# Optimization experiments

Measured on AMD Instinct MI355X. Metric: run time of the kernel, lower is better.

The kernel has to match this reference:

```python
import jax, jax.numpy as jnp
import numpy as np

NUM_QUBITS = 4
NUM_LAYERS = 3


def _ry(state, theta, wire):
    # state: (N,2,2,2,2) real amplitudes; RY(theta) on `wire` (angle scalar or (N,))
    st = jnp.moveaxis(state, wire + 1, -1)
    c = jnp.cos(theta * 0.5)
    s = jnp.sin(theta * 0.5)
    if jnp.ndim(c) == 1:  # per-sample angle -> broadcast over remaining qubit axes
        shape = (c.shape[0],) + (1,) * (st.ndim - 2)
        c = c.reshape(shape)
        s = s.reshape(shape)
    s0, s1 = st[..., 0], st[..., 1]
    new = jnp.stack([c * s0 - s * s1, s * s0 + c * s1], axis=-1)
    return jnp.moveaxis(new, -1, wire + 1)


def _cnot(state, control, target):
    st = jnp.moveaxis(state, (control + 1, target + 1), (-2, -1))
    new = jnp.stack([st[..., 0, :], st[..., 1, ::-1]], axis=-2)
    return jnp.moveaxis(new, (-2, -1), (control + 1, target + 1))


def _circuit(angles, params):
    # angles: (N,4) input rotations; params: (L,4,1) shared variational angles
    N = angles.shape[0]
    state = jnp.zeros((N, 2, 2, 2, 2), angles.dtype).at[:, 0, 0, 0, 0].set(1.0)
    for q in range(NUM_QUBITS):
        state = _ry(state, angles[:, q], q)
    for l in range(NUM_LAYERS):
        for q in range(NUM_QUBITS):
            state = _ry(state, params[l, q, 0], q)
        for q in range(NUM_QUBITS - 1):
            state = _cnot(state, q, q + 1)
    probs = state * state  # amplitudes are real (only RY/CNOT)
    meas = []
    for w in range(NUM_QUBITS):
        axes = tuple(a for a in range(1, NUM_QUBITS + 1) if a != w + 1)
        p = probs.sum(axes)  # (N,2)
        meas.append(p[:, 0] - p[:, 1])  # <Z_w>
    return jnp.stack(meas, axis=-1)  # (N,4)


def setup_inputs() -> dict:
    key = jax.random.key(0)
    k1, k2, k3, k4, k5 = jax.random.split(key, 5)
    B = 8192
    return {
        "x": jax.random.uniform(k1, (B, 1, 28, 28), dtype=jnp.float32),
        "params": jax.random.normal(k2, (NUM_LAYERS, NUM_QUBITS, 1), dtype=jnp.float32),
        "res_w": jax.random.normal(k3, (4, 1, 1, 1), dtype=jnp.float32),
        "cls_w": jax.random.normal(k4, (10, 784), dtype=jnp.float32) * 0.03,
        "cls_b": jax.random.normal(k5, (10,), dtype=jnp.float32) * 0.03,
    }


def reference(x, params, res_w, cls_w, cls_b):
    B = x.shape[0]
    img = x.reshape(B, 28, 28)
    # extract 2x2 patches, element order (r,c),(r,c+1),(r+1,c),(r+1,c+1)
    patches = img.reshape(B, 14, 2, 14, 2).transpose(0, 1, 3, 2, 4).reshape(B, 196, 4)
    # per-patch-index min/max over batch and the 4 elements (matches patch.min()/max())
    mn = patches.min(axis=(0, 2), keepdims=True)
    mx = patches.max(axis=(0, 2), keepdims=True)
    ang = (patches - mn) / (mx - mn + 1e-8) * jnp.pi
    meas = _circuit(ang.reshape(B * 196, 4), params)  # (B*196, 4)
    out = meas.reshape(B, 196 * 4).reshape(B, 4, 14, 14)  # matches torch.cat(...).view
    # res_conv: 1x1 conv, stride 2, no bias -> strided pixel scaled per out-channel
    res = img[:, ::2, ::2][:, None, :, :] * res_w.reshape(1, 4, 1, 1)
    out = out + res
    logits = out.reshape(B, -1) @ cls_w.T + cls_b
    return jax.nn.log_softmax(logits, axis=-1)
```

## Files before the change

### kernel.cpp

```cpp
#include <hip/hip_runtime.h>
#include <math.h>

#define NP 196
#define PI_F 3.14159265358979323846f

__device__ __forceinline__ unsigned fkey(float f) {
  unsigned u = __float_as_uint(f);
  return u ^ ((unsigned)((int)u >> 31) | 0x80000000u);
}
__device__ __forceinline__ float funkey(unsigned k) {
  unsigned u = (k & 0x80000000u) ? (k ^ 0x80000000u) : ~k;
  return __uint_as_float(u);
}

__global__ void __launch_bounds__(256) precompute_kernel(
    const float* __restrict__ params, const float* __restrict__ res_w,
    const float* __restrict__ cls_w, float* __restrict__ U,
    float* __restrict__ W2, unsigned* __restrict__ mn,
    unsigned* __restrict__ mx) {
  const int tid = threadIdx.x;
  if (tid < NP) {
    mn[tid] = 0xFFFFFFFFu;
    mx[tid] = 0u;
  }
  if (tid < 16) {
    float cp[12], sp[12];
#pragma unroll
    for (int l = 0; l < 12; ++l) __sincosf(0.5f * params[l], &sp[l], &cp[l]);
    float st[16];
#pragma unroll
    for (int i = 0; i < 16; ++i) st[i] = 0.f;
    st[tid] = 1.f;
#pragma unroll
    for (int l = 0; l < 3; ++l) {
#pragma unroll
      for (int q = 0; q < 4; ++q) {
        const float cq = cp[l * 4 + q], sq = sp[l * 4 + q];
        const int m = 8 >> q;
#pragma unroll
        for (int idx = 0; idx < 16; ++idx) {
          if (idx & m) continue;
          float v0 = st[idx], v1 = st[idx | m];
          st[idx] = cq * v0 - sq * v1;
          st[idx | m] = sq * v0 + cq * v1;
        }
      }
#pragma unroll
      for (int q = 0; q < 3; ++q) {
        const int mc = 8 >> q, mt = 4 >> q;
#pragma unroll
        for (int idx = 0; idx < 16; ++idx) {
          if ((idx & mc) && !(idx & mt)) {
            float t0 = st[idx];
            st[idx] = st[idx | mt];
            st[idx | mt] = t0;
          }
        }
      }
    }
#pragma unroll
    for (int i = 0; i < 16; ++i) U[i * 16 + tid] = st[i];
  }
  for (int t = tid; t < 10 * NP; t += 256) {
    int k = t / NP, p = t - k * NP;
    float s = 0.f;
#pragma unroll
    for (int c = 0; c < 4; ++c) s += res_w[c] * cls_w[k * 784 + c * NP + p];
    W2[t] = s;
  }
}

__global__ void __launch_bounds__(512) minmax_kernel(
    const float* __restrict__ x, unsigned* __restrict__ mn,
    unsigned* __restrict__ mx, int imgs, int B) {
  __shared__ unsigned skmin[392], skmax[392];
  const int t = threadIdx.x;
  const int img0 = blockIdx.x * imgs;
  if (t < 392) {
    const int r = t / 14, j = t - r * 14;
    const float* base = x + (size_t)img0 * 784 + r * 28 + 2 * j;
    const int nimg = (img0 + imgs <= B) ? imgs : (B - img0);
    float lmn0 = 3.4e38f, lmn1 = 3.4e38f;
    float lmx0 = -3.4e38f, lmx1 = -3.4e38f;
    int m = 0;
#pragma unroll 4
    for (; m + 1 < nimg; m += 2) {
      float2 v0 = *(const float2*)(base + (size_t)m * 784);
      float2 v1 = *(const float2*)(base + (size_t)(m + 1) * 784);
      lmn0 = fminf(lmn0, fminf(v0.x, v0.y));
      lmx0 = fmaxf(lmx0, fmaxf(v0.x, v0.y));
      lmn1 = fminf(lmn1, fminf(v1.x, v1.y));
      lmx1 = fmaxf(lmx1, fmaxf(v1.x, v1.y));
    }
    if (m < nimg) {
      float2 v0 = *(const float2*)(base + (size_t)m * 784);
      lmn0 = fminf(lmn0, fminf(v0.x, v0.y));
      lmx0 = fmaxf(lmx0, fmaxf(v0.x, v0.y));
    }
    skmin[t] = fkey(fminf(lmn0, lmn1));
    skmax[t] = fkey(fmaxf(lmx0, lmx1));
  }
  __syncthreads();
  if (t < NP) {
    const int i = t / 14, j = t - i * 14;
    const int f0 = (2 * i) * 14 + j, f1 = f0 + 14;
    unsigned kmn = skmin[f0] < skmin[f1] ? skmin[f0] : skmin[f1];
    unsigned kmx = skmax[f0] > skmax[f1] ? skmax[f0] : skmax[f1];
    atomicMin(&mn[t], kmn);
    atomicMax(&mx[t], kmx);
  }
}

__global__ void __launch_bounds__(256) fused_kernel(
    const float* __restrict__ x, const unsigned* __restrict__ mnk,
    const unsigned* __restrict__ mxk, const float* __restrict__ U,
    const float* __restrict__ W2, const float* __restrict__ cls_w,
    const float* __restrict__ cls_b, float* __restrict__ out) {
  __shared__ float partial[4][10];

  const int t = threadIdx.x;
  const int b = blockIdx.x;

  float acc[10];
#pragma unroll
  for (int k = 0; k < 10; ++k) acc[k] = 0.f;

  if (t < NP) {
    const int p = t;
    const int i = p / 14, j = p - i * 14;
    const float* px = x + (size_t)b * 784 + (2 * i) * 28 + 2 * j;
    const float2 r0 = *(const float2*)px;
    const float2 r1 = *(const float2*)(px + 28);

    const float mnv = funkey(mnk[p]);
    const float mxv = funkey(mxk[p]);
    const float sc = (0.5f * PI_F) / (mxv - mnv + 1e-8f);

    float cc[4], ss[4];
    __sincosf((r0.x - mnv) * sc, &ss[0], &cc[0]);
    __sincosf((r0.y - mnv) * sc, &ss[1], &cc[1]);
    __sincosf((r1.x - mnv) * sc, &ss[2], &cc[2]);
    __sincosf((r1.y - mnv) * sc, &ss[3], &cc[3]);

    float st0[16];
    {
      const float A[4] = {cc[0] * cc[1], cc[0] * ss[1], ss[0] * cc[1], ss[0] * ss[1]};
      const float Bq[4] = {cc[2] * cc[3], cc[2] * ss[3], ss[2] * cc[3], ss[2] * ss[3]};
#pragma unroll
      for (int idx = 0; idx < 16; ++idx) st0[idx] = A[idx >> 2] * Bq[idx & 3];
    }

    float a8[8], z3 = 0.f;
#pragma unroll
    for (int k = 0; k < 8; ++k) {
      float f0 = 0.f, f1 = 0.f;
#pragma unroll
      for (int jx = 0; jx < 16; ++jx) {
        f0 = fmaf(U[(2 * k) * 16 + jx], st0[jx], f0);
        f1 = fmaf(U[(2 * k + 1) * 16 + jx], st0[jx], f1);
      }
      const float s0 = f0 * f0, s1 = f1 * f1;
      a8[k] = s0 + s1;
      z3 += s0 - s1;
    }
    float bb[4], z2 = 0.f;
#pragma unroll
    for (int k = 0; k < 4; ++k) {
      bb[k] = a8[2 * k] + a8[2 * k + 1];
      z2 += a8[2 * k] - a8[2 * k + 1];
    }
    const float e0 = bb[0] + bb[1], e1 = bb[2] + bb[3];
    const float z1 = (bb[0] - bb[1]) + (bb[2] - bb[3]);
    const float z0 = e0 - e1;
    const float v = r0.x;

#pragma unroll
    for (int k = 0; k < 10; ++k) {
      const float4 w4 = *(const float4*)(cls_w + k * 784 + 4 * p);
      float a = z0 * w4.x;
      a = fmaf(z1, w4.y, a);
      a = fmaf(z2, w4.z, a);
      a = fmaf(z3, w4.w, a);
      acc[k] = fmaf(v, W2[k * NP + p], a);
    }
  }

  const int lane = t & 63, wv = t >> 6;
#pragma unroll
  for (int k = 0; k < 10; ++k) {
    float a = acc[k];
#pragma unroll
    for (int off = 32; off > 0; off >>= 1) a += __shfl_down(a, off, 64);
    if (lane == 0) partial[wv][k] = a;
  }
  __syncthreads();

  if (t == 0) {
    float lg[10];
#pragma unroll
    for (int k = 0; k < 10; ++k)
      lg[k] = partial[0][k] + partial[1][k] + partial[2][k] + partial[3][k] + cls_b[k];
    float m = lg[0];
#pragma unroll
    for (int k = 1; k < 10; ++k) m = fmaxf(m, lg[k]);
    float s = 0.f;
#pragma unroll
    for (int k = 0; k < 10; ++k) s += __expf(lg[k] - m);
    const float lse = m + __logf(s);
#pragma unroll
    for (int k = 0; k < 10; ++k) out[(size_t)b * 10 + k] = lg[k] - lse;
  }
}

extern "C" void kernel_launch(void* const* d_in, const int* in_sizes, int n_in,
                              void* d_out, int out_size, void* d_ws, size_t ws_size,
                              hipStream_t stream) {
  const float* x      = (const float*)d_in[0];
  const float* params = (const float*)d_in[1];
  const float* res_w  = (const float*)d_in[2];
  const float* cls_w  = (const float*)d_in[3];
  const float* cls_b  = (const float*)d_in[4];
  float* out = (float*)d_out;
  const int B = in_sizes[0] / 784;

  unsigned* mn = (unsigned*)d_ws;
  unsigned* mx = mn + NP;
  float* U  = (float*)(mx + NP);
  float* W2 = U + 256;

  precompute_kernel<<<1, 256, 0, stream>>>(params, res_w, cls_w, U, W2, mn, mx);

  const int imgs = 16;
  const int nblk1 = (B + imgs - 1) / imgs;
  minmax_kernel<<<nblk1, 512, 0, stream>>>(x, mn, mx, imgs, B);

  fused_kernel<<<B, 256, 0, stream>>>(x, mn, mx, U, W2, cls_w, cls_b, out);
}
```

Before: 127.1 us.

## Map one image per wavefront in fused kernel, dropping block barrier

The fused kernel now gives each 64-lane wavefront one image and loops over the 196 patches in four strided passes, instead of one 256-thread block per image with 60 idle threads. The cross-wave shared-memory reduction and __syncthreads are removed, since the wave-level shuffle reduction alone yields the logits. The grid shrinks by 4x. This raises lane utilisation and removes the barrier, at the cost of a serial loop per wave (the last pass is mostly idle) and fewer independent blocks.

```diff
diff --git a/kernel.cpp b/kernel.cpp
--- a/kernel.cpp
+++ b/kernel.cpp
@@ -115,91 +115,93 @@
     const float* __restrict__ x, const unsigned* __restrict__ mnk,
     const unsigned* __restrict__ mxk, const float* __restrict__ U,
     const float* __restrict__ W2, const float* __restrict__ cls_w,
-    const float* __restrict__ cls_b, float* __restrict__ out) {
-  __shared__ float partial[4][10];
-
-  const int t = threadIdx.x;
-  const int b = blockIdx.x;
+    const float* __restrict__ cls_b, float* __restrict__ out, int B) {
+  const int lane = threadIdx.x & 63;
+  const int wv = threadIdx.x >> 6;
+  const int b = blockIdx.x * 4 + wv;
+  if (b >= B) return;
+
+  const float* ximg = x + (size_t)b * 784;
 
   float acc[10];
 #pragma unroll
   for (int k = 0; k < 10; ++k) acc[k] = 0.f;
 
-  if (t < NP) {
-    const int p = t;
-    const int i = p / 14, j = p - i * 14;
-    const float* px = x + (size_t)b * 784 + (2 * i) * 28 + 2 * j;
-    const float2 r0 = *(const float2*)px;
-    const float2 r1 = *(const float2*)(px + 28);
-
-    const float mnv = funkey(mnk[p]);
-    const float mxv = funkey(mxk[p]);
-    const float sc = (0.5f * PI_F) / (mxv - mnv + 1e-8f);
-
-    float cc[4], ss[4];
-    __sincosf((r0.x - mnv) * sc, &ss[0], &cc[0]);
-    __sincosf((r0.y - mnv) * sc, &ss[1], &cc[1]);
-    __sincosf((r1.x - mnv) * sc, &ss[2], &cc[2]);
-    __sincosf((r1.y - mnv) * sc, &ss[3], &cc[3]);
-
-    float st0[16];
-    {
-      const float A[4] = {cc[0] * cc[1], cc[0] * ss[1], ss[0] * cc[1], ss[0] * ss[1]};
-      const float Bq[4] = {cc[2] * cc[3], cc[2] * ss[3], ss[2] * cc[3], ss[2] * ss[3]};
-#pragma unroll
-      for (int idx = 0; idx < 16; ++idx) st0[idx] = A[idx >> 2] * Bq[idx & 3];
-    }
-
-    float a8[8], z3 = 0.f;
-#pragma unroll
-    for (int k = 0; k < 8; ++k) {
-      float f0 = 0.f, f1 = 0.f;
-#pragma unroll
-      for (int jx = 0; jx < 16; ++jx) {
-        f0 = fmaf(U[(2 * k) * 16 + jx], st0[jx], f0);
-        f1 = fmaf(U[(2 * k + 1) * 16 + jx], st0[jx], f1);
-      }
-      const float s0 = f0 * f0, s1 = f1 * f1;
-      a8[k] = s0 + s1;
-      z3 += s0 - s1;
-    }
-    float bb[4], z2 = 0.f;
-#pragma unroll
-    for (int k = 0; k < 4; ++k) {
-      bb[k] = a8[2 * k] + a8[2 * k + 1];
-      z2 += a8[2 * k] - a8[2 * k + 1];
-    }
-    const float e0 = bb[0] + bb[1], e1 = bb[2] + bb[3];
-    const float z1 = (bb[0] - bb[1]) + (bb[2] - bb[3]);
-    const float z0 = e0 - e1;
-    const float v = r0.x;
-
-#pragma unroll
-    for (int k = 0; k < 10; ++k) {
-      const float4 w4 = *(const float4*)(cls_w + k * 784 + 4 * p);
-      float a = z0 * w4.x;
-      a = fmaf(z1, w4.y, a);
-      a = fmaf(z2, w4.z, a);
-      a = fmaf(z3, w4.w, a);
-      acc[k] = fmaf(v, W2[k * NP + p], a);
-    }
-  }
-
-  const int lane = t & 63, wv = t >> 6;
+#pragma unroll 1
+  for (int it = 0; it < 4; ++it) {
+    const int p = it * 64 + lane;
+    if (p < NP) {
+      const int i = p / 14, j = p - i * 14;
+      const float* px = ximg + (2 * i) * 28 + 2 * j;
+      const float2 r0 = *(const float2*)px;
+      const float2 r1 = *(const float2*)(px + 28);
+
+      const float mnv = funkey(mnk[p]);
+      const float mxv = funkey(mxk[p]);
+      const float sc = (0.5f * PI_F) / (mxv - mnv + 1e-8f);
+
+      float cc[4], ss[4];
+      __sincosf((r0.x - mnv) * sc, &ss[0], &cc[0]);
+      __sincosf((r0.y - mnv) * sc, &ss[1], &cc[1]);
+      __sincosf((r1.x - mnv) * sc, &ss[2], &cc[2]);
+      __sincosf((r1.y - mnv) * sc, &ss[3], &cc[3]);
+
+      float st0[16];
+      {
+        const float A[4] = {cc[0] * cc[1], cc[0] * ss[1], ss[0] * cc[1], ss[0] * ss[1]};
+        const float Bq[4] = {cc[2] * cc[3], cc[2] * ss[3], ss[2] * cc[3], ss[2] * ss[3]};
+#pragma unroll
+        for (int idx = 0; idx < 16; ++idx) st0[idx] = A[idx >> 2] * Bq[idx & 3];
+      }
+
+      float a8[8], z3 = 0.f;
+#pragma unroll
+      for (int k = 0; k < 8; ++k) {
+        float f0 = 0.f, f1 = 0.f;
+#pragma unroll
+        for (int jx = 0; jx < 16; ++jx) {
+          f0 = fmaf(U[(2 * k) * 16 + jx], st0[jx], f0);
+          f1 = fmaf(U[(2 * k + 1) * 16 + jx], st0[jx], f1);
+        }
+        const float s0 = f0 * f0, s1 = f1 * f1;
+        a8[k] = s0 + s1;
+        z3 += s0 - s1;
+      }
+      float bb[4], z2 = 0.f;
+#pragma unroll
+      for (int k = 0; k < 4; ++k) {
+        bb[k] = a8[2 * k] + a8[2 * k + 1];
+        z2 += a8[2 * k] - a8[2 * k + 1];
+      }
+      const float e0 = bb[0] + bb[1], e1 = bb[2] + bb[3];
+      const float z1 = (bb[0] - bb[1]) + (bb[2] - bb[3]);
+      const float z0 = e0 - e1;
+      const float v = r0.x;
+
+#pragma unroll
+      for (int k = 0; k < 10; ++k) {
+        const float4 w4 = *(const float4*)(cls_w + k * 784 + 4 * p);
+        float a = z0 * w4.x;
+        a = fmaf(z1, w4.y, a);
+        a = fmaf(z2, w4.z, a);
+        a = fmaf(z3, w4.w, a);
+        acc[k] += fmaf(v, W2[k * NP + p], a);
+      }
+    }
+  }
+
 #pragma unroll
   for (int k = 0; k < 10; ++k) {
     float a = acc[k];
 #pragma unroll
     for (int off = 32; off > 0; off >>= 1) a += __shfl_down(a, off, 64);
-    if (lane == 0) partial[wv][k] = a;
-  }
-  __syncthreads();
-
-  if (t == 0) {
+    acc[k] = a;
+  }
+
+  if (lane == 0) {
     float lg[10];
 #pragma unroll
-    for (int k = 0; k < 10; ++k)
-      lg[k] = partial[0][k] + partial[1][k] + partial[2][k] + partial[3][k] + cls_b[k];
+    for (int k = 0; k < 10; ++k) lg[k] = acc[k] + cls_b[k];
     float m = lg[0];
 #pragma unroll
     for (int k = 1; k < 10; ++k) m = fmaxf(m, lg[k]);
@@ -234,5 +236,6 @@
   const int nblk1 = (B + imgs - 1) / imgs;
   minmax_kernel<<<nblk1, 512, 0, stream>>>(x, mn, mx, imgs, B);
 
-  fused_kernel<<<B, 256, 0, stream>>>(x, mn, mx, U, W2, cls_w, cls_b, out);
-}
+  const int nblk2 = (B + 3) / 4;
+  fused_kernel<<<nblk2, 256, 0, stream>>>(x, mn, mx, U, W2, cls_w, cls_b, out, B);
+}
```

After: 123.9 us. 2.5% less time.
